# Kernel tuning notes

Measured on AMD Instinct MI355X. Metric: run time of the kernel, lower is better.

Reference implementation:

```python
import jax, jax.numpy as jnp
import numpy as np

DIM = 1024
HEADS = 16
HEAD_DIM = DIM // HEADS
B, T = 2, 2048


def setup_inputs() -> dict:
    key = jax.random.key(0)
    ks = jax.random.split(key, 6)
    x = jax.random.normal(ks[0], (B, T, DIM), dtype=jnp.float32)
    # Linear weights stored as [in, out] for x @ W + b
    w_qkv = jax.random.normal(ks[1], (DIM, 3 * DIM), dtype=jnp.float32) * (1.0 / np.sqrt(DIM))
    b_qkv = jnp.zeros((3 * DIM,), dtype=jnp.float32)
    w_out = jax.random.normal(ks[2], (DIM, DIM), dtype=jnp.float32) * (1.0 / np.sqrt(DIM))
    b_out = jnp.zeros((DIM,), dtype=jnp.float32)
    pos_bias = jax.random.normal(ks[3], (1, HEADS, 1, HEAD_DIM), dtype=jnp.float32) * 0.1
    return {"x": x, "w_qkv": w_qkv, "b_qkv": b_qkv, "w_out": w_out, "b_out": b_out, "pos_bias": pos_bias}


def reference(x, w_qkv, b_qkv, w_out, b_out, pos_bias):
    b, t, c = x.shape
    scale = HEAD_DIM ** -0.5
    qkv = x @ w_qkv + b_qkv                       # [B, T, 3C]
    q, k, v = jnp.split(qkv, 3, axis=-1)
    # [B, T, C] -> [B, H, T, Dh]
    def to_heads(z):
        return z.reshape(b, t, HEADS, HEAD_DIM).transpose(0, 2, 1, 3)
    q = to_heads(q) + pos_bias                    # learned query positional bias
    k = to_heads(k)
    v = to_heads(v)
    attn = jnp.einsum('bhqd,bhkd->bhqk', q, k) * scale
    causal = jnp.tril(jnp.ones((t, t), dtype=bool))
    attn = jnp.where(causal[None, None], attn, -jnp.inf)
    attn = jax.nn.softmax(attn, axis=-1)
    out = jnp.einsum('bhqk,bhkd->bhqd', attn, v)  # [B, H, T, Dh]
    out = out.transpose(0, 2, 1, 3).reshape(b, t, c)
    # dropout inactive (eval mode)
    return out @ w_out + b_out
```

## Files before the change

kernel.cpp:

```cpp
#include <hip/hip_runtime.h>

#define DIM 1024
#define HEADS 16
#define HD 64
#define BATCH 2
#define SEQ 2048
#define MROWS (BATCH*SEQ)
#define NQKV (3*DIM)
#define BK 32
#define NT (DIM/BK)
#define ALDT 72

typedef unsigned short u16;
typedef __attribute__((ext_vector_type(8))) short short8;
typedef __attribute__((ext_vector_type(4))) float f32x4;

#define QSCALE 0.1803368801111204f
#define DTHR 11.5f

__device__ __forceinline__ u16 f2bf(float f) {
  unsigned u = __float_as_uint(f);
  u += 0x7FFFu + ((u >> 16) & 1u);
  return (u16)(u >> 16);
}

__device__ __forceinline__ void gload16(const u16* g, u16* l) {
  __builtin_amdgcn_global_load_lds((const __attribute__((address_space(1))) unsigned int*)g,
                                   (__attribute__((address_space(3))) unsigned int*)l, 16, 0, 0);
}

__global__ void k_f32_to_bf16(const float* __restrict__ in, u16* __restrict__ out, int n8) {
  int i = blockIdx.x * blockDim.x + threadIdx.x;
  if (i >= n8) return;
  const float4* p = (const float4*)in + (size_t)i * 2;
  float4 a = p[0], b = p[1];
  short8 v;
  v[0] = (short)f2bf(a.x); v[1] = (short)f2bf(a.y);
  v[2] = (short)f2bf(a.z); v[3] = (short)f2bf(a.w);
  v[4] = (short)f2bf(b.x); v[5] = (short)f2bf(b.y);
  v[6] = (short)f2bf(b.z); v[7] = (short)f2bf(b.w);
  ((short8*)out)[i] = v;
}

__global__ void k_transpose2(const float* __restrict__ wqkv, u16* __restrict__ oqkv,
                             const float* __restrict__ wout, u16* __restrict__ oout) {
  __shared__ float tile[32][33];
  const int bx = blockIdx.x;
  const float* in; u16* out; int C, c0;
  if (bx < 96) { in = wqkv; out = oqkv; C = NQKV; c0 = bx * 32; }
  else         { in = wout; out = oout; C = DIM;  c0 = (bx - 96) * 32; }
  const int r0 = blockIdx.y * 32;
  const int tx = threadIdx.x, ty = threadIdx.y;
#pragma unroll
  for (int i = 0; i < 4; ++i)
    tile[ty + 8 * i][tx] = in[(size_t)(r0 + ty + 8 * i) * C + c0 + tx];
  __syncthreads();
#pragma unroll
  for (int i = 0; i < 4; ++i)
    out[(size_t)(c0 + ty + 8 * i) * DIM + r0 + tx] = f2bf(tile[tx][ty + 8 * i]);
}

#define GEMM_PREAMBLE(Aptr, Bptr)                                              \
  __shared__ u16 lds_[3 * 8192];                                               \
  const int tid = threadIdx.x;                                                 \
  const int lane = tid & 63;                                                   \
  const int wid = tid >> 6;                                                    \
  const int wm = wid >> 1, wn = wid & 1;                                       \
  const int rowA0 = blockIdx.y * 128;                                          \
  const int rowB0 = blockIdx.x * 128;                                          \
  const int rl = lane & 15, lg = lane >> 4;                                    \
  const int csw = (rl >> 1) & 3;                                               \
  const f32x4 fz = {0.f, 0.f, 0.f, 0.f};                                       \
  f32x4 acc[4][4];                                                             \
  _Pragma("unroll") for (int i = 0; i < 4; ++i)                                \
  _Pragma("unroll") for (int j = 0; j < 4; ++j) acc[i][j] = fz;                \
  const int srow = tid >> 2;                                                   \
  const int scol = ((tid & 3) ^ ((tid >> 3) & 3)) * 8;                         \
  const u16* gA = (Aptr) + (size_t)(rowA0 + srow) * DIM + scol;                \
  const u16* gB = (Bptr) + (size_t)(rowB0 + srow) * DIM + scol;                \
  auto stage = [&](int t, int j) {                                             \
    u16* d = lds_ + j * 8192;                                                  \
    gload16(gA + t * BK, d + tid * 8);                                         \
    gload16(gA + (size_t)64 * DIM + t * BK, d + 2048 + tid * 8);               \
    gload16(gB + t * BK, d + 4096 + tid * 8);                                  \
    gload16(gB + (size_t)64 * DIM + t * BK, d + 6144 + tid * 8);               \
  };                                                                           \
  auto compute = [&](int j) {                                                  \
    const u16* bufA = lds_ + j * 8192;                                         \
    const u16* bufB = bufA + 4096;                                             \
    short8 af[4], bfr[4];                                                      \
    _Pragma("unroll") for (int mf = 0; mf < 4; ++mf)                           \
      af[mf] = *(const short8*)(bufA + (wm * 64 + mf * 16 + rl) * 32 +         \
                                ((lg ^ csw) * 8));                             \
    _Pragma("unroll") for (int nf = 0; nf < 4; ++nf)                           \
      bfr[nf] = *(const short8*)(bufB + (wn * 64 + nf * 16 + rl) * 32 +        \
                                 ((lg ^ csw) * 8));                            \
    __builtin_amdgcn_s_setprio(1);                                             \
    _Pragma("unroll") for (int mf = 0; mf < 4; ++mf)                           \
    _Pragma("unroll") for (int nf = 0; nf < 4; ++nf)                           \
      acc[mf][nf] =                                                            \
          __builtin_amdgcn_mfma_f32_16x16x32_bf16(af[mf], bfr[nf],             \
                                                  acc[mf][nf], 0, 0, 0);       \
    __builtin_amdgcn_s_setprio(0);                                             \
  };                                                                           \
  stage(0, 0);                                                                 \
  stage(1, 1);                                                                 \
  asm volatile("s_waitcnt vmcnt(4)" ::: "memory");                             \
  __builtin_amdgcn_s_barrier();                                                \
  int cur = 0;                                                                 \
  _Pragma("unroll 3") for (int t = 0; t < NT - 2; ++t) {                       \
    int nb = cur + 2; if (nb >= 3) nb -= 3;                                    \
    stage(t + 2, nb);                                                          \
    compute(cur);                                                              \
    asm volatile("s_waitcnt vmcnt(4)" ::: "memory");                           \
    __builtin_amdgcn_s_barrier();                                              \
    cur = cur + 1; if (cur == 3) cur = 0;                                      \
  }                                                                            \
  compute(cur);                                                                \
  asm volatile("s_waitcnt vmcnt(0)" ::: "memory");                             \
  __builtin_amdgcn_s_barrier();                                                \
  cur = cur + 1; if (cur == 3) cur = 0;                                        \
  compute(cur);

__global__ __launch_bounds__(256) void k_gemm_qkv(
    const u16* __restrict__ A, const u16* __restrict__ Bt,
    const float* __restrict__ bias, const float* __restrict__ posb,
    u16* __restrict__ qb, u16* __restrict__ kb, u16* __restrict__ vtb) {
  GEMM_PREAMBLE(A, Bt)

#pragma unroll
  for (int mf = 0; mf < 4; ++mf) {
#pragma unroll
    for (int nf = 0; nf < 4; ++nf) {
#pragma unroll
      for (int r = 0; r < 4; ++r) {
        const int row = rowA0 + wm * 64 + mf * 16 + lg * 4 + r;
        const int col = rowB0 + wn * 64 + nf * 16 + rl;
        float v = acc[mf][nf][r] + bias[col];
        const int which = col >> 10;
        const int within = col & 1023;
        const int h = within >> 6, d = within & 63;
        const int bb = row >> 11, t = row & 2047;
        const size_t bh = (size_t)(bb * HEADS + h);
        if (which == 0) {
          v = (v + posb[within]) * QSCALE;
          qb[(bh * SEQ + t) * HD + d] = f2bf(v);
        } else if (which == 1) {
          kb[(bh * SEQ + t) * HD + d] = f2bf(v);
        } else {
          vtb[(bh * HD + d) * SEQ + t] = f2bf(v);
        }
      }
    }
  }
}

__global__ __launch_bounds__(256) void k_gemm_out(
    const u16* __restrict__ A, const u16* __restrict__ Bt,
    const float* __restrict__ bias, float* __restrict__ out) {
  GEMM_PREAMBLE(A, Bt)

#pragma unroll
  for (int mf = 0; mf < 4; ++mf)
#pragma unroll
    for (int nf = 0; nf < 4; ++nf)
#pragma unroll
      for (int r = 0; r < 4; ++r) {
        const int row = rowA0 + wm * 64 + mf * 16 + lg * 4 + r;
        const int col = rowB0 + wn * 64 + nf * 16 + rl;
        out[(size_t)row * DIM + col] = acc[mf][nf][r] + bias[col];
      }
}

__global__ __launch_bounds__(256) void k_attn(
    const u16* __restrict__ qg, const u16* __restrict__ kg, const u16* __restrict__ vg,
    u16* __restrict__ og) {
  __shared__ u16 lK[64 * ALDT];
  __shared__ u16 lV[64 * ALDT];
  const int tid = threadIdx.x;
  const int lane = tid & 63;
  const int wid = tid >> 6;
  const int rl = lane & 15, lg = lane >> 4;
  const int bh = blockIdx.x & 31;
  const int qt = blockIdx.x >> 5;
  const int b = bh >> 4, h = bh & 15;

  const u16* gK = kg + (size_t)bh * SEQ * HD;
  const u16* gV = vg + (size_t)bh * HD * SEQ;
  const int sr = tid >> 3;
  const int sc = (tid & 7) * 8;
  const int sl0 = (((2 * lg) & 3) << 4) + rl;
  const int sl1 = (((2 * lg + 1) & 3) << 4) + rl;
  const bool hi = (lg >= 2);

  const int qrow = qt * 64 + wid * 16 + rl;
  const u16* qptr = qg + ((size_t)bh * SEQ + qrow) * HD + lg * 8;
  const short8 aq0 = *(const short8*)(qptr);
  const short8 aq1 = *(const short8*)(qptr + 32);

  const f32x4 fz = {0.f, 0.f, 0.f, 0.f};
  f32x4 o[4];
#pragma unroll
  for (int dt = 0; dt < 4; ++dt) o[dt] = fz;
  float m = -1e30f, l = 0.f;

  int4 rka = *(const int4*)(gK + (size_t)sr * HD + sc);
  int4 rkb = *(const int4*)(gK + (size_t)(sr + 32) * HD + sc);
  int4 rva = *(const int4*)(gV + (size_t)sr * SEQ + sc);
  int4 rvb = *(const int4*)(gV + (size_t)(sr + 32) * SEQ + sc);

  for (int kt = 0; kt <= qt; ++kt) {
    __syncthreads();
    *(int4*)(lK + sr * ALDT + sc) = rka;
    *(int4*)(lK + (sr + 32) * ALDT + sc) = rkb;
    *(int4*)(lV + sr * ALDT + sc) = rva;
    *(int4*)(lV + (sr + 32) * ALDT + sc) = rvb;
    __syncthreads();
    if (kt < qt) {
      const int kv1 = (kt + 1) * 64;
      rka = *(const int4*)(gK + (size_t)(kv1 + sr) * HD + sc);
      rkb = *(const int4*)(gK + (size_t)(kv1 + sr + 32) * HD + sc);
      rva = *(const int4*)(gV + (size_t)sr * SEQ + kv1 + sc);
      rvb = *(const int4*)(gV + (size_t)(sr + 32) * SEQ + kv1 + sc);
    }

    f32x4 s[4];
#pragma unroll
    for (int ct = 0; ct < 4; ++ct) s[ct] = fz;
    __builtin_amdgcn_s_setprio(1);
#pragma unroll
    for (int ct = 0; ct < 4; ++ct) {
      short8 ak0 = *(const short8*)(lK + (ct * 16 + rl) * ALDT + lg * 8);
      short8 ak1 = *(const short8*)(lK + (ct * 16 + rl) * ALDT + 32 + lg * 8);
      s[ct] = __builtin_amdgcn_mfma_f32_16x16x32_bf16(ak0, aq0, s[ct], 0, 0, 0);
      s[ct] = __builtin_amdgcn_mfma_f32_16x16x32_bf16(ak1, aq1, s[ct], 0, 0, 0);
    }
    __builtin_amdgcn_s_setprio(0);

    if (kt == qt) {
#pragma unroll
      for (int ct = 0; ct < 4; ++ct)
#pragma unroll
        for (int r = 0; r < 4; ++r)
          if (kt * 64 + ct * 16 + lg * 4 + r > qrow) s[ct][r] = -1e30f;
    }

    float cm[4];
#pragma unroll
    for (int ct = 0; ct < 4; ++ct)
      cm[ct] = fmaxf(fmaxf(s[ct][0], s[ct][1]), fmaxf(s[ct][2], s[ct][3]));
    float pmax = fmaxf(fmaxf(cm[0], cm[1]), fmaxf(cm[2], cm[3]));
    pmax = fmaxf(pmax, __shfl_xor(pmax, 16, 64));
    pmax = fmaxf(pmax, __shfl_xor(pmax, 32, 64));

    if (__any(pmax - m > DTHR)) {
      const float mn = fmaxf(m, pmax);
      const float alpha = __builtin_amdgcn_exp2f(m - mn);
      m = mn;
      l *= alpha;
#pragma unroll
      for (int dt = 0; dt < 4; ++dt)
#pragma unroll
        for (int r = 0; r < 4; ++r) o[dt][r] *= alpha;
    }

    float rc[4];
    unsigned pk[4][2];
#pragma unroll
    for (int ct = 0; ct < 4; ++ct) {
      float p0 = __builtin_amdgcn_exp2f(s[ct][0] - m);
      float p1 = __builtin_amdgcn_exp2f(s[ct][1] - m);
      float p2 = __builtin_amdgcn_exp2f(s[ct][2] - m);
      float p3 = __builtin_amdgcn_exp2f(s[ct][3] - m);
      rc[ct] = (p0 + p1) + (p2 + p3);
      pk[ct][0] = (unsigned)f2bf(p0) | ((unsigned)f2bf(p1) << 16);
      pk[ct][1] = (unsigned)f2bf(p2) | ((unsigned)f2bf(p3) << 16);
    }
    l += (rc[0] + rc[1]) + (rc[2] + rc[3]);

#pragma unroll
    for (int kb2 = 0; kb2 < 2; ++kb2) {
      unsigned a0 = (unsigned)__shfl((int)pk[2 * kb2 + 0][0], sl0, 64);
      unsigned b0 = (unsigned)__shfl((int)pk[2 * kb2 + 1][0], sl0, 64);
      unsigned a1 = (unsigned)__shfl((int)pk[2 * kb2 + 0][1], sl0, 64);
      unsigned b1 = (unsigned)__shfl((int)pk[2 * kb2 + 1][1], sl0, 64);
      unsigned a2 = (unsigned)__shfl((int)pk[2 * kb2 + 0][0], sl1, 64);
      unsigned b2 = (unsigned)__shfl((int)pk[2 * kb2 + 1][0], sl1, 64);
      unsigned a3 = (unsigned)__shfl((int)pk[2 * kb2 + 0][1], sl1, 64);
      unsigned b3 = (unsigned)__shfl((int)pk[2 * kb2 + 1][1], sl1, 64);
      union { unsigned u[4]; short8 s8; } pu;
      pu.u[0] = hi ? b0 : a0;
      pu.u[1] = hi ? b1 : a1;
      pu.u[2] = hi ? b2 : a2;
      pu.u[3] = hi ? b3 : a3;
      __builtin_amdgcn_s_setprio(1);
#pragma unroll
      for (int dt = 0; dt < 4; ++dt) {
        short8 av = *(const short8*)(lV + (dt * 16 + rl) * ALDT + kb2 * 32 + lg * 8);
        o[dt] = __builtin_amdgcn_mfma_f32_16x16x32_bf16(av, pu.s8, o[dt], 0, 0, 0);
      }
      __builtin_amdgcn_s_setprio(0);
    }
  }

  l += __shfl_xor(l, 16, 64);
  l += __shfl_xor(l, 32, 64);
  const float linv = __builtin_amdgcn_rcpf(l);
  const size_t obase = ((size_t)b * SEQ + qrow) * DIM + h * HD;
#pragma unroll
  for (int dt = 0; dt < 4; ++dt) {
    union { u16 e[4]; uint2 v; } w;
    w.e[0] = f2bf(o[dt][0] * linv);
    w.e[1] = f2bf(o[dt][1] * linv);
    w.e[2] = f2bf(o[dt][2] * linv);
    w.e[3] = f2bf(o[dt][3] * linv);
    *(uint2*)(og + obase + dt * 16 + lg * 4) = w.v;
  }
}

extern "C" void kernel_launch(void* const* d_in, const int* in_sizes, int n_in,
                              void* d_out, int out_size, void* d_ws, size_t ws_size,
                              hipStream_t stream) {
  const float* x = (const float*)d_in[0];
  const float* w_qkv = (const float*)d_in[1];
  const float* b_qkv = (const float*)d_in[2];
  const float* w_out = (const float*)d_in[3];
  const float* b_out = (const float*)d_in[4];
  const float* pos_bias = (const float*)d_in[5];
  float* out = (float*)d_out;

  u16* ws = (u16*)d_ws;
  u16* xb = ws;
  u16* wqkvb = xb + (size_t)MROWS * DIM;
  u16* woutb = wqkvb + (size_t)NQKV * DIM;
  u16* qb = woutb + (size_t)DIM * DIM;
  u16* kbuf = qb + (size_t)BATCH * HEADS * SEQ * HD;
  u16* vtb = kbuf + (size_t)BATCH * HEADS * SEQ * HD;
  u16* attnb = xb;

  k_f32_to_bf16<<<(MROWS * DIM / 8 + 255) / 256, 256, 0, stream>>>(x, xb, MROWS * DIM / 8);
  k_transpose2<<<dim3(128, DIM / 32), dim3(32, 8), 0, stream>>>(w_qkv, wqkvb, w_out, woutb);
  k_gemm_qkv<<<dim3(NQKV / 128, MROWS / 128), 256, 0, stream>>>(xb, wqkvb, b_qkv, pos_bias, qb, kbuf, vtb);
  k_attn<<<dim3(BATCH * HEADS * 32), 256, 0, stream>>>(qb, kbuf, vtb, attnb);
  k_gemm_out<<<dim3(DIM / 128, MROWS / 128), 256, 0, stream>>>(attnb, woutb, b_out, out);
}
```

Measured before the change: 211.5 us.

## Pair causal attention tiles per block and retile output GEMM to 128x64

The attention kernel now gives each block two query tiles, one from the end and one from the start of the sequence (31-p and p), so every block does the same amount of causal work, and the grid is halved. The output projection GEMM switches to a 128x64 tile with its own triple-buffered LDS pipeline and swizzled layout, which doubles its block count to 512 and should fill the CUs better. The intent is to remove load imbalance in the causal attention and the low occupancy of the output GEMM. The cost is fewer attention blocks, 512, each running two passes in sequence, and extra per-block overhead in the GEMM.

```diff
diff --git a/kernel.cpp b/kernel.cpp
--- a/kernel.cpp
+++ b/kernel.cpp
@@ -158,16 +158,77 @@
 __global__ __launch_bounds__(256) void k_gemm_out(
     const u16* __restrict__ A, const u16* __restrict__ Bt,
     const float* __restrict__ bias, float* __restrict__ out) {
-  GEMM_PREAMBLE(A, Bt)
+  __shared__ u16 lds_[3 * 6144];
+  const int tid = threadIdx.x;
+  const int lane = tid & 63;
+  const int wid = tid >> 6;
+  const int wm = wid >> 1, wn = wid & 1;
+  const int rowA0 = blockIdx.y * 128;
+  const int rowB0 = blockIdx.x * 64;
+  const int rl = lane & 15, lg = lane >> 4;
+  const int csw = (rl >> 1) & 3;
+  const f32x4 fz = {0.f, 0.f, 0.f, 0.f};
+  f32x4 acc[4][2];
+#pragma unroll
+  for (int i = 0; i < 4; ++i)
+#pragma unroll
+    for (int j = 0; j < 2; ++j) acc[i][j] = fz;
+  const int srow = tid >> 2;
+  const int scol = ((tid & 3) ^ ((tid >> 3) & 3)) * 8;
+  const u16* gA = A + (size_t)(rowA0 + srow) * DIM + scol;
+  const u16* gB = Bt + (size_t)(rowB0 + srow) * DIM + scol;
+  auto stage = [&](int t, int j) {
+    u16* d = lds_ + j * 6144;
+    gload16(gA + t * BK, d + tid * 8);
+    gload16(gA + (size_t)64 * DIM + t * BK, d + 2048 + tid * 8);
+    gload16(gB + t * BK, d + 4096 + tid * 8);
+  };
+  auto compute = [&](int j) {
+    const u16* bufA = lds_ + j * 6144;
+    const u16* bufB = bufA + 4096;
+    short8 af[4], bfr[2];
+#pragma unroll
+    for (int mf = 0; mf < 4; ++mf)
+      af[mf] = *(const short8*)(bufA + (wm * 64 + mf * 16 + rl) * 32 + ((lg ^ csw) * 8));
+#pragma unroll
+    for (int nf = 0; nf < 2; ++nf)
+      bfr[nf] = *(const short8*)(bufB + (wn * 32 + nf * 16 + rl) * 32 + ((lg ^ csw) * 8));
+    __builtin_amdgcn_s_setprio(1);
+#pragma unroll
+    for (int mf = 0; mf < 4; ++mf)
+#pragma unroll
+      for (int nf = 0; nf < 2; ++nf)
+        acc[mf][nf] = __builtin_amdgcn_mfma_f32_16x16x32_bf16(af[mf], bfr[nf], acc[mf][nf], 0, 0, 0);
+    __builtin_amdgcn_s_setprio(0);
+  };
+  stage(0, 0);
+  stage(1, 1);
+  asm volatile("s_waitcnt vmcnt(3)" ::: "memory");
+  __builtin_amdgcn_s_barrier();
+  int cur = 0;
+#pragma unroll 3
+  for (int t = 0; t < NT - 2; ++t) {
+    int nb = cur + 2; if (nb >= 3) nb -= 3;
+    stage(t + 2, nb);
+    compute(cur);
+    asm volatile("s_waitcnt vmcnt(3)" ::: "memory");
+    __builtin_amdgcn_s_barrier();
+    cur = cur + 1; if (cur == 3) cur = 0;
+  }
+  compute(cur);
+  asm volatile("s_waitcnt vmcnt(0)" ::: "memory");
+  __builtin_amdgcn_s_barrier();
+  cur = cur + 1; if (cur == 3) cur = 0;
+  compute(cur);
 
 #pragma unroll
   for (int mf = 0; mf < 4; ++mf)
 #pragma unroll
-    for (int nf = 0; nf < 4; ++nf)
+    for (int nf = 0; nf < 2; ++nf)
 #pragma unroll
       for (int r = 0; r < 4; ++r) {
         const int row = rowA0 + wm * 64 + mf * 16 + lg * 4 + r;
-        const int col = rowB0 + wn * 64 + nf * 16 + rl;
+        const int col = rowB0 + wn * 32 + nf * 16 + rl;
         out[(size_t)row * DIM + col] = acc[mf][nf][r] + bias[col];
       }
 }
@@ -182,7 +243,7 @@
   const int wid = tid >> 6;
   const int rl = lane & 15, lg = lane >> 4;
   const int bh = blockIdx.x & 31;
-  const int qt = blockIdx.x >> 5;
+  const int pair = blockIdx.x >> 5;
   const int b = bh >> 4, h = bh & 15;
 
   const u16* gK = kg + (size_t)bh * SEQ * HD;
@@ -193,128 +254,132 @@
   const int sl1 = (((2 * lg + 1) & 3) << 4) + rl;
   const bool hi = (lg >= 2);
 
-  const int qrow = qt * 64 + wid * 16 + rl;
-  const u16* qptr = qg + ((size_t)bh * SEQ + qrow) * HD + lg * 8;
-  const short8 aq0 = *(const short8*)(qptr);
-  const short8 aq1 = *(const short8*)(qptr + 32);
-
-  const f32x4 fz = {0.f, 0.f, 0.f, 0.f};
-  f32x4 o[4];
-#pragma unroll
-  for (int dt = 0; dt < 4; ++dt) o[dt] = fz;
-  float m = -1e30f, l = 0.f;
-
-  int4 rka = *(const int4*)(gK + (size_t)sr * HD + sc);
-  int4 rkb = *(const int4*)(gK + (size_t)(sr + 32) * HD + sc);
-  int4 rva = *(const int4*)(gV + (size_t)sr * SEQ + sc);
-  int4 rvb = *(const int4*)(gV + (size_t)(sr + 32) * SEQ + sc);
-
-  for (int kt = 0; kt <= qt; ++kt) {
-    __syncthreads();
-    *(int4*)(lK + sr * ALDT + sc) = rka;
-    *(int4*)(lK + (sr + 32) * ALDT + sc) = rkb;
-    *(int4*)(lV + sr * ALDT + sc) = rva;
-    *(int4*)(lV + (sr + 32) * ALDT + sc) = rvb;
-    __syncthreads();
-    if (kt < qt) {
-      const int kv1 = (kt + 1) * 64;
-      rka = *(const int4*)(gK + (size_t)(kv1 + sr) * HD + sc);
-      rkb = *(const int4*)(gK + (size_t)(kv1 + sr + 32) * HD + sc);
-      rva = *(const int4*)(gV + (size_t)sr * SEQ + kv1 + sc);
-      rvb = *(const int4*)(gV + (size_t)(sr + 32) * SEQ + kv1 + sc);
+#pragma unroll 1
+  for (int half = 0; half < 2; ++half) {
+    const int qt = half ? pair : (31 - pair);
+    const int qrow = qt * 64 + wid * 16 + rl;
+    const u16* qptr = qg + ((size_t)bh * SEQ + qrow) * HD + lg * 8;
+    const short8 aq0 = *(const short8*)(qptr);
+    const short8 aq1 = *(const short8*)(qptr + 32);
+
+    const f32x4 fz = {0.f, 0.f, 0.f, 0.f};
+    f32x4 o[4];
+#pragma unroll
+    for (int dt = 0; dt < 4; ++dt) o[dt] = fz;
+    float m = -1e30f, l = 0.f;
+
+    int4 rka = *(const int4*)(gK + (size_t)sr * HD + sc);
+    int4 rkb = *(const int4*)(gK + (size_t)(sr + 32) * HD + sc);
+    int4 rva = *(const int4*)(gV + (size_t)sr * SEQ + sc);
+    int4 rvb = *(const int4*)(gV + (size_t)(sr + 32) * SEQ + sc);
+
+    for (int kt = 0; kt <= qt; ++kt) {
+      __syncthreads();
+      *(int4*)(lK + sr * ALDT + sc) = rka;
+      *(int4*)(lK + (sr + 32) * ALDT + sc) = rkb;
+      *(int4*)(lV + sr * ALDT + sc) = rva;
+      *(int4*)(lV + (sr + 32) * ALDT + sc) = rvb;
+      __syncthreads();
+      if (kt < qt) {
+        const int kv1 = (kt + 1) * 64;
+        rka = *(const int4*)(gK + (size_t)(kv1 + sr) * HD + sc);
+        rkb = *(const int4*)(gK + (size_t)(kv1 + sr + 32) * HD + sc);
+        rva = *(const int4*)(gV + (size_t)sr * SEQ + kv1 + sc);
+        rvb = *(const int4*)(gV + (size_t)(sr + 32) * SEQ + kv1 + sc);
+      }
+
+      f32x4 s[4];
+#pragma unroll
+      for (int ct = 0; ct < 4; ++ct) s[ct] = fz;
+      __builtin_amdgcn_s_setprio(1);
+#pragma unroll
+      for (int ct = 0; ct < 4; ++ct) {
+        short8 ak0 = *(const short8*)(lK + (ct * 16 + rl) * ALDT + lg * 8);
+        short8 ak1 = *(const short8*)(lK + (ct * 16 + rl) * ALDT + 32 + lg * 8);
+        s[ct] = __builtin_amdgcn_mfma_f32_16x16x32_bf16(ak0, aq0, s[ct], 0, 0, 0);
+        s[ct] = __builtin_amdgcn_mfma_f32_16x16x32_bf16(ak1, aq1, s[ct], 0, 0, 0);
+      }
+      __builtin_amdgcn_s_setprio(0);
+
+      if (kt == qt) {
+#pragma unroll
+        for (int ct = 0; ct < 4; ++ct)
+#pragma unroll
+          for (int r = 0; r < 4; ++r)
+            if (kt * 64 + ct * 16 + lg * 4 + r > qrow) s[ct][r] = -1e30f;
+      }
+
+      float cm[4];
+#pragma unroll
+      for (int ct = 0; ct < 4; ++ct)
+        cm[ct] = fmaxf(fmaxf(s[ct][0], s[ct][1]), fmaxf(s[ct][2], s[ct][3]));
+      float pmax = fmaxf(fmaxf(cm[0], cm[1]), fmaxf(cm[2], cm[3]));
+      pmax = fmaxf(pmax, __shfl_xor(pmax, 16, 64));
+      pmax = fmaxf(pmax, __shfl_xor(pmax, 32, 64));
+
+      if (__any(pmax - m > DTHR)) {
+        const float mn = fmaxf(m, pmax);
+        const float alpha = __builtin_amdgcn_exp2f(m - mn);
+        m = mn;
+        l *= alpha;
+#pragma unroll
+        for (int dt = 0; dt < 4; ++dt)
+#pragma unroll
+          for (int r = 0; r < 4; ++r) o[dt][r] *= alpha;
+      }
+
+      float rc[4];
+      unsigned pk[4][2];
+#pragma unroll
+      for (int ct = 0; ct < 4; ++ct) {
+        float p0 = __builtin_amdgcn_exp2f(s[ct][0] - m);
+        float p1 = __builtin_amdgcn_exp2f(s[ct][1] - m);
+        float p2 = __builtin_amdgcn_exp2f(s[ct][2] - m);
+        float p3 = __builtin_amdgcn_exp2f(s[ct][3] - m);
+        rc[ct] = (p0 + p1) + (p2 + p3);
+        pk[ct][0] = (unsigned)f2bf(p0) | ((unsigned)f2bf(p1) << 16);
+        pk[ct][1] = (unsigned)f2bf(p2) | ((unsigned)f2bf(p3) << 16);
+      }
+      l += (rc[0] + rc[1]) + (rc[2] + rc[3]);
+
+#pragma unroll
+      for (int kb2 = 0; kb2 < 2; ++kb2) {
+        unsigned a0 = (unsigned)__shfl((int)pk[2 * kb2 + 0][0], sl0, 64);
+        unsigned b0 = (unsigned)__shfl((int)pk[2 * kb2 + 1][0], sl0, 64);
+        unsigned a1 = (unsigned)__shfl((int)pk[2 * kb2 + 0][1], sl0, 64);
+        unsigned b1 = (unsigned)__shfl((int)pk[2 * kb2 + 1][1], sl0, 64);
+        unsigned a2 = (unsigned)__shfl((int)pk[2 * kb2 + 0][0], sl1, 64);
+        unsigned b2 = (unsigned)__shfl((int)pk[2 * kb2 + 1][0], sl1, 64);
+        unsigned a3 = (unsigned)__shfl((int)pk[2 * kb2 + 0][1], sl1, 64);
+        unsigned b3 = (unsigned)__shfl((int)pk[2 * kb2 + 1][1], sl1, 64);
+        union { unsigned u[4]; short8 s8; } pu;
+        pu.u[0] = hi ? b0 : a0;
+        pu.u[1] = hi ? b1 : a1;
+        pu.u[2] = hi ? b2 : a2;
+        pu.u[3] = hi ? b3 : a3;
+        __builtin_amdgcn_s_setprio(1);
+#pragma unroll
+        for (int dt = 0; dt < 4; ++dt) {
+          short8 av = *(const short8*)(lV + (dt * 16 + rl) * ALDT + kb2 * 32 + lg * 8);
+          o[dt] = __builtin_amdgcn_mfma_f32_16x16x32_bf16(av, pu.s8, o[dt], 0, 0, 0);
+        }
+        __builtin_amdgcn_s_setprio(0);
+      }
     }
 
-    f32x4 s[4];
-#pragma unroll
-    for (int ct = 0; ct < 4; ++ct) s[ct] = fz;
-    __builtin_amdgcn_s_setprio(1);
-#pragma unroll
-    for (int ct = 0; ct < 4; ++ct) {
-      short8 ak0 = *(const short8*)(lK + (ct * 16 + rl) * ALDT + lg * 8);
-      short8 ak1 = *(const short8*)(lK + (ct * 16 + rl) * ALDT + 32 + lg * 8);
-      s[ct] = __builtin_amdgcn_mfma_f32_16x16x32_bf16(ak0, aq0, s[ct], 0, 0, 0);
-      s[ct] = __builtin_amdgcn_mfma_f32_16x16x32_bf16(ak1, aq1, s[ct], 0, 0, 0);
+    l += __shfl_xor(l, 16, 64);
+    l += __shfl_xor(l, 32, 64);
+    const float linv = __builtin_amdgcn_rcpf(l);
+    const size_t obase = ((size_t)b * SEQ + qrow) * DIM + h * HD;
+#pragma unroll
+    for (int dt = 0; dt < 4; ++dt) {
+      union { u16 e[4]; uint2 v; } w;
+      w.e[0] = f2bf(o[dt][0] * linv);
+      w.e[1] = f2bf(o[dt][1] * linv);
+      w.e[2] = f2bf(o[dt][2] * linv);
+      w.e[3] = f2bf(o[dt][3] * linv);
+      *(uint2*)(og + obase + dt * 16 + lg * 4) = w.v;
     }
-    __builtin_amdgcn_s_setprio(0);
-
-    if (kt == qt) {
-#pragma unroll
-      for (int ct = 0; ct < 4; ++ct)
-#pragma unroll
-        for (int r = 0; r < 4; ++r)
-          if (kt * 64 + ct * 16 + lg * 4 + r > qrow) s[ct][r] = -1e30f;
-    }
-
-    float cm[4];
-#pragma unroll
-    for (int ct = 0; ct < 4; ++ct)
-      cm[ct] = fmaxf(fmaxf(s[ct][0], s[ct][1]), fmaxf(s[ct][2], s[ct][3]));
-    float pmax = fmaxf(fmaxf(cm[0], cm[1]), fmaxf(cm[2], cm[3]));
-    pmax = fmaxf(pmax, __shfl_xor(pmax, 16, 64));
-    pmax = fmaxf(pmax, __shfl_xor(pmax, 32, 64));
-
-    if (__any(pmax - m > DTHR)) {
-      const float mn = fmaxf(m, pmax);
-      const float alpha = __builtin_amdgcn_exp2f(m - mn);
-      m = mn;
-      l *= alpha;
-#pragma unroll
-      for (int dt = 0; dt < 4; ++dt)
-#pragma unroll
-        for (int r = 0; r < 4; ++r) o[dt][r] *= alpha;
-    }
-
-    float rc[4];
-    unsigned pk[4][2];
-#pragma unroll
-    for (int ct = 0; ct < 4; ++ct) {
-      float p0 = __builtin_amdgcn_exp2f(s[ct][0] - m);
-      float p1 = __builtin_amdgcn_exp2f(s[ct][1] - m);
-      float p2 = __builtin_amdgcn_exp2f(s[ct][2] - m);
-      float p3 = __builtin_amdgcn_exp2f(s[ct][3] - m);
-      rc[ct] = (p0 + p1) + (p2 + p3);
-      pk[ct][0] = (unsigned)f2bf(p0) | ((unsigned)f2bf(p1) << 16);
-      pk[ct][1] = (unsigned)f2bf(p2) | ((unsigned)f2bf(p3) << 16);
-    }
-    l += (rc[0] + rc[1]) + (rc[2] + rc[3]);
-
-#pragma unroll
-    for (int kb2 = 0; kb2 < 2; ++kb2) {
-      unsigned a0 = (unsigned)__shfl((int)pk[2 * kb2 + 0][0], sl0, 64);
-      unsigned b0 = (unsigned)__shfl((int)pk[2 * kb2 + 1][0], sl0, 64);
-      unsigned a1 = (unsigned)__shfl((int)pk[2 * kb2 + 0][1], sl0, 64);
-      unsigned b1 = (unsigned)__shfl((int)pk[2 * kb2 + 1][1], sl0, 64);
-      unsigned a2 = (unsigned)__shfl((int)pk[2 * kb2 + 0][0], sl1, 64);
-      unsigned b2 = (unsigned)__shfl((int)pk[2 * kb2 + 1][0], sl1, 64);
-      unsigned a3 = (unsigned)__shfl((int)pk[2 * kb2 + 0][1], sl1, 64);
-      unsigned b3 = (unsigned)__shfl((int)pk[2 * kb2 + 1][1], sl1, 64);
-      union { unsigned u[4]; short8 s8; } pu;
-      pu.u[0] = hi ? b0 : a0;
-      pu.u[1] = hi ? b1 : a1;
-      pu.u[2] = hi ? b2 : a2;
-      pu.u[3] = hi ? b3 : a3;
-      __builtin_amdgcn_s_setprio(1);
-#pragma unroll
-      for (int dt = 0; dt < 4; ++dt) {
-        short8 av = *(const short8*)(lV + (dt * 16 + rl) * ALDT + kb2 * 32 + lg * 8);
-        o[dt] = __builtin_amdgcn_mfma_f32_16x16x32_bf16(av, pu.s8, o[dt], 0, 0, 0);
-      }
-      __builtin_amdgcn_s_setprio(0);
-    }
-  }
-
-  l += __shfl_xor(l, 16, 64);
-  l += __shfl_xor(l, 32, 64);
-  const float linv = __builtin_amdgcn_rcpf(l);
-  const size_t obase = ((size_t)b * SEQ + qrow) * DIM + h * HD;
-#pragma unroll
-  for (int dt = 0; dt < 4; ++dt) {
-    union { u16 e[4]; uint2 v; } w;
-    w.e[0] = f2bf(o[dt][0] * linv);
-    w.e[1] = f2bf(o[dt][1] * linv);
-    w.e[2] = f2bf(o[dt][2] * linv);
-    w.e[3] = f2bf(o[dt][3] * linv);
-    *(uint2*)(og + obase + dt * 16 + lg * 4) = w.v;
   }
 }
 
@@ -341,6 +406,6 @@
   k_f32_to_bf16<<<(MROWS * DIM / 8 + 255) / 256, 256, 0, stream>>>(x, xb, MROWS * DIM / 8);
   k_transpose2<<<dim3(128, DIM / 32), dim3(32, 8), 0, stream>>>(w_qkv, wqkvb, w_out, woutb);
   k_gemm_qkv<<<dim3(NQKV / 128, MROWS / 128), 256, 0, stream>>>(xb, wqkvb, b_qkv, pos_bias, qb, kbuf, vtb);
-  k_attn<<<dim3(BATCH * HEADS * 32), 256, 0, stream>>>(qb, kbuf, vtb, attnb);
-  k_gemm_out<<<dim3(DIM / 128, MROWS / 128), 256, 0, stream>>>(attnb, woutb, b_out, out);
-}
+  k_attn<<<dim3(BATCH * HEADS * 16), 256, 0, stream>>>(qb, kbuf, vtb, attnb);
+  k_gemm_out<<<dim3(DIM / 64, MROWS / 128), 256, 0, stream>>>(attnb, woutb, b_out, out);
+}
```

Measured after the change: 203.3 us. 1.04x faster.
